# Kernel optimization log

Measured on AMD Instinct MI355X. Metric: run time of the kernel, lower is better.

## Reference

```python
import jax, jax.numpy as jnp
import numpy as np

HIDDEN = 768
HEAD = 64


def setup_inputs() -> dict:
    key = jax.random.key(0)
    ks = jax.random.split(key, 9)
    s = 1.0 / np.sqrt(HIDDEN)
    so = 1.0 / np.sqrt(HEAD)
    return {
        "x": jax.random.normal(ks[0], (4, 4096, HIDDEN), dtype=jnp.float32),
        "Wq": jax.random.uniform(ks[1], (HIDDEN, HEAD), jnp.float32, -s, s),
        "bq": jax.random.uniform(ks[2], (HEAD,), jnp.float32, -s, s),
        "Wk": jax.random.uniform(ks[3], (HIDDEN, HEAD), jnp.float32, -s, s),
        "bk": jax.random.uniform(ks[4], (HEAD,), jnp.float32, -s, s),
        "Wv": jax.random.uniform(ks[5], (HIDDEN, HEAD), jnp.float32, -s, s),
        "bv": jax.random.uniform(ks[6], (HEAD,), jnp.float32, -s, s),
        "Wo": jax.random.uniform(ks[7], (HEAD, HIDDEN), jnp.float32, -so, so),
        "bo": jax.random.uniform(ks[8], (HIDDEN,), jnp.float32, -so, so),
    }


def reference(x, Wq, bq, Wk, bk, Wv, bv, Wo, bo):
    # x: [b, s, h]
    q = jnp.einsum('bsh,hd->bsd', x, Wq) + bq  # [b, s, d]
    k = jnp.einsum('bsh,hd->bsd', x, Wk) + bk
    v = jnp.einsum('bsh,hd->bsd', x, Wv) + bv
    scale = 1.0 / jnp.sqrt(jnp.asarray(HEAD, x.dtype))
    scores = jnp.einsum('bqd,bkd->bqk', q, k) * scale  # [b, s, s]
    A = jax.nn.softmax(scores, axis=-1)
    ctx = jnp.einsum('bqk,bkd->bqd', A, v)  # [b, s, d]
    return jnp.einsum('bsd,dh->bsh', ctx, Wo) + bo
```

## Files before the change

kernel.cpp:

```cpp
#include <hip/hip_runtime.h>
#include <hip/hip_bf16.h>
#include <stdint.h>

#define BB 4
#define SS 4096
#define HH 768
#define DD 64

typedef __attribute__((ext_vector_type(8))) short bf16x8;
typedef __attribute__((ext_vector_type(4))) short bf16x4;
typedef __attribute__((ext_vector_type(4))) float f32x4;
typedef __attribute__((ext_vector_type(2))) float f32x2;
typedef __attribute__((ext_vector_type(16))) float f32x16;
typedef __attribute__((ext_vector_type(4))) uint32_t u32x4;
typedef __attribute__((ext_vector_type(2))) uint32_t u32x2;

typedef const __attribute__((address_space(1))) uint32_t g_u32;
typedef __attribute__((address_space(3))) uint32_t l_u32;
#define ASYNC16(gp, lp) \
  __builtin_amdgcn_global_load_lds((g_u32*)(gp), (l_u32*)(lp), 16, 0, 0)

__device__ __forceinline__ short f2bf(float f) {
  uint32_t u = __builtin_bit_cast(uint32_t, f);
  u += 0x7fffu + ((u >> 16) & 1u);
  return (short)(u >> 16);
}

#define QSCALE 0.18033688011112042f

__global__ __launch_bounds__(256) void prep_kernel(
    const float* __restrict__ Wq, const float* __restrict__ bq,
    const float* __restrict__ Wk, const float* __restrict__ bk,
    const float* __restrict__ Wv, const float* __restrict__ bv,
    const float* __restrict__ Wo,
    short* __restrict__ wqkvF, float* __restrict__ bqkv,
    short* __restrict__ woF) {
  int idx = blockIdx.x * 256 + threadIdx.x;
  const int N1 = 192 * HH;
  const int N2 = HH * DD;
  if (idx < N1) {
    int n = idx / HH, k = idx % HH;
    float v;
    if (n < 64)       v = Wq[k * 64 + n] * QSCALE;
    else if (n < 128) v = Wk[k * 64 + (n - 64)];
    else              v = Wv[k * 64 + (n - 128)];
    int tile = (n >> 4) * 24 + (k >> 5);
    int lane = (((k >> 3) & 3) << 4) | (n & 15);
    wqkvF[tile * 512 + lane * 8 + (k & 7)] = f2bf(v);
  } else if (idx < N1 + N2) {
    int j = idx - N1;
    int n = j / 64, k = j % 64;
    int tile = (n >> 4) * 2 + (k >> 5);
    int lane = (((k >> 3) & 3) << 4) | (n & 15);
    woF[tile * 512 + lane * 8 + (k & 7)] = f2bf(Wo[k * HH + n]);
  } else if (idx < N1 + N2 + 192) {
    int n = idx - N1 - N2;
    float v;
    if (n < 64)       v = bq[n] * QSCALE;
    else if (n < 128) v = bk[n - 64];
    else              v = bv[n - 128];
    bqkv[n] = v;
  }
}

__global__ __launch_bounds__(256, 2) void qkv_kernel(
    const float* __restrict__ x, const short* __restrict__ wF,
    const float* __restrict__ bqkv,
    short* __restrict__ qb, short* __restrict__ kb, short* __restrict__ vT) {
  __shared__ short xl[32 * 776];
  __shared__ short vtile[64 * 32];
  const int tid = threadIdx.x;
  const int w = tid >> 6, lane = tid & 63, g = (lane >> 4) & 3, n16 = lane & 15;
  const int m0 = blockIdx.x * 32;

  const float4* xsrc = (const float4*)&x[m0 * HH];
#pragma unroll
  for (int i = 0; i < 24; ++i) {
    int idx = i * 256 + tid;
    const float4 f = xsrc[idx];
    int elem = idx * 4;
    int row = elem / HH, col = elem % HH;
    bf16x4 p = { f2bf(f.x), f2bf(f.y), f2bf(f.z), f2bf(f.w) };
    *(bf16x4*)&xl[row * 776 + col] = p;
  }
  __syncthreads();

  f32x4 acc[2][3] = {};
  const short* wbase = &wF[w * 36864 + lane * 8];

#pragma unroll 2
  for (int kc = 0; kc < 24; ++kc) {
    const int ko = kc * 32 + g * 8;
    bf16x8 a0 = *(const bf16x8*)&xl[n16 * 776 + ko];
    bf16x8 a1 = *(const bf16x8*)&xl[(16 + n16) * 776 + ko];
    bf16x8 b0 = *(const bf16x8*)&wbase[kc * 512];
    bf16x8 b1 = *(const bf16x8*)&wbase[12288 + kc * 512];
    bf16x8 b2 = *(const bf16x8*)&wbase[24576 + kc * 512];
    acc[0][0] = __builtin_amdgcn_mfma_f32_16x16x32_bf16(a0, b0, acc[0][0], 0, 0, 0);
    acc[1][0] = __builtin_amdgcn_mfma_f32_16x16x32_bf16(a1, b0, acc[1][0], 0, 0, 0);
    acc[0][1] = __builtin_amdgcn_mfma_f32_16x16x32_bf16(a0, b1, acc[0][1], 0, 0, 0);
    acc[1][1] = __builtin_amdgcn_mfma_f32_16x16x32_bf16(a1, b1, acc[1][1], 0, 0, 0);
    acc[0][2] = __builtin_amdgcn_mfma_f32_16x16x32_bf16(a0, b2, acc[0][2], 0, 0, 0);
    acc[1][2] = __builtin_amdgcn_mfma_f32_16x16x32_bf16(a1, b2, acc[1][2], 0, 0, 0);
  }

#pragma unroll
  for (int ct = 0; ct < 3; ++ct) {
    int nG = w * 48 + ct * 16 + n16;
    float bias = bqkv[nG];
    if (nG < 128) {
#pragma unroll
      for (int rt = 0; rt < 2; ++rt)
#pragma unroll
        for (int r = 0; r < 4; ++r) {
          int rowg = m0 + rt * 16 + g * 4 + r;
          short val = f2bf(acc[rt][ct][r] + bias);
          if (nG < 64) qb[rowg * 64 + nG] = val;
          else         kb[rowg * 64 + (nG - 64)] = val;
        }
    } else {
      int d = nG - 128;
#pragma unroll
      for (int rt = 0; rt < 2; ++rt) {
        bf16x4 p = { f2bf(acc[rt][ct][0] + bias), f2bf(acc[rt][ct][1] + bias),
                     f2bf(acc[rt][ct][2] + bias), f2bf(acc[rt][ct][3] + bias) };
        *(bf16x4*)&vtile[d * 32 + rt * 16 + g * 4] = p;
      }
    }
  }

  __syncthreads();
  {
    int d = tid >> 2, part = tid & 3;
    bf16x8 o = *(const bf16x8*)&vtile[d * 32 + part * 8];
    int b = m0 >> 12;
    *(bf16x8*)&vT[(b * 64 + d) * SS + (m0 & 4095) + part * 8] = o;
  }
}

__global__ __launch_bounds__(256, 2) void flash_kernel(
    const short* __restrict__ qb, const short* __restrict__ kb,
    const short* __restrict__ vT,
    float* __restrict__ Opart, float* __restrict__ lpart) {
  __shared__ short Kl[2][128 * 64];
  __shared__ short Vl[2][64 * 128];
  __shared__ float l_lds[64];
  const int tid = threadIdx.x;
  const int w = tid >> 6, lane = tid & 63;
  const int m31 = lane & 31, h = lane >> 5;
  const int qt32 = w & 1, kh = w >> 1;
  const int part = blockIdx.x, rg = part >> 1, sp = part & 1;
  const int b = rg >> 6, qt = rg & 63;
  const short* qB = qb + (b * SS + qt * 64 + qt32 * 32) * DD;
  const short* kB = kb + (b * SS + sp * 2048) * DD;
  const short* vB = vT + b * DD * SS + sp * 2048;

  int srcK[4], srcV[4];
#pragma unroll
  for (int i = 0; i < 4; ++i) {
    int rowK = (w * 4 + i) * 8 + (lane >> 3);
    srcK[i] = rowK * 64 + (((lane & 7) ^ (rowK & 7)) << 3);
    int dV = (w * 4 + i) * 4 + (lane >> 4);
    srcV[i] = dV * SS + (((lane & 15) ^ (dV & 15)) << 3);
  }

  bf16x8 aQ[4];
#pragma unroll
  for (int kk = 0; kk < 4; ++kk)
    aQ[kk] = *(const bf16x8*)&qB[m31 * DD + kk * 16 + 8 * h];

  f32x16 oacc[2] = {};
  float l_run = 0.f;

#pragma unroll
  for (int i = 0; i < 4; ++i) {
    ASYNC16(kB + srcK[i], &Kl[0][(w * 4 + i) * 512]);
    ASYNC16(vB + srcV[i], &Vl[0][(w * 4 + i) * 512]);
  }

  for (int kt = 0; kt < 16; ++kt) {
    const int cur = kt & 1;
    if (kt < 15) {
      const short* kN = kB + (kt + 1) * 8192;
      const short* vN = vB + (kt + 1) * 128;
#pragma unroll
      for (int i = 0; i < 4; ++i) {
        ASYNC16(kN + srcK[i], &Kl[cur ^ 1][(w * 4 + i) * 512]);
        ASYNC16(vN + srcV[i], &Vl[cur ^ 1][(w * 4 + i) * 512]);
      }
      asm volatile("s_waitcnt vmcnt(8)" ::: "memory");
    } else {
      asm volatile("s_waitcnt vmcnt(0)" ::: "memory");
    }
    __builtin_amdgcn_s_barrier();
    __builtin_amdgcn_sched_barrier(0);

#pragma unroll
    for (int kt2 = 0; kt2 < 2; ++kt2) {
      f32x16 sc = {};
      const int r = kh * 64 + kt2 * 32 + m31;
      const int rx = r & 7;
      __builtin_amdgcn_s_setprio(1);
#pragma unroll
      for (int kk = 0; kk < 4; ++kk) {
        bf16x8 aK = *(const bf16x8*)&Kl[cur][r * 64 + ((((kk << 1) | h) ^ rx) << 3)];
        sc = __builtin_amdgcn_mfma_f32_32x32x16_bf16(aK, aQ[kk], sc, 0, 0, 0);
      }
      __builtin_amdgcn_s_setprio(0);

      f32x2 ls2 = {0.f, 0.f};
      uint32_t pp[8];
#pragma unroll
      for (int j = 0; j < 8; ++j) {
        uint32_t ea = __builtin_bit_cast(uint32_t,
                        __builtin_amdgcn_exp2f(sc[2 * j]));
        uint32_t eb = __builtin_bit_cast(uint32_t,
                        __builtin_amdgcn_exp2f(sc[2 * j + 1]));
        f32x2 t = { __builtin_bit_cast(float, ea & 0xffff0000u),
                    __builtin_bit_cast(float, eb & 0xffff0000u) };
        ls2 += t;
        pp[j] = __builtin_amdgcn_perm(eb, ea, 0x07060302u);
      }
      l_run += ls2.x + ls2.y;

      u32x2 r02 = __builtin_amdgcn_permlane32_swap(pp[0], pp[2], false, false);
      u32x2 r13 = __builtin_amdgcn_permlane32_swap(pp[1], pp[3], false, false);
      u32x2 r46 = __builtin_amdgcn_permlane32_swap(pp[4], pp[6], false, false);
      u32x2 r57 = __builtin_amdgcn_permlane32_swap(pp[5], pp[7], false, false);

#pragma unroll
      for (int s = 0; s < 2; ++s) {
        u32x4 fr = (s == 0) ? u32x4{r02.x, r13.x, r02.y, r13.y}
                            : u32x4{r46.x, r57.x, r46.y, r57.y};
        bf16x8 aP = __builtin_bit_cast(bf16x8, fr);
        const int cv = (kh << 3) | (kt2 << 2) | (s << 1) | h;
        __builtin_amdgcn_s_setprio(1);
#pragma unroll
        for (int dt = 0; dt < 2; ++dt) {
          const int rv = dt * 32 + m31;
          bf16x8 bV = *(const bf16x8*)&Vl[cur][rv * 128 + ((cv ^ (rv & 15)) << 3)];
          oacc[dt] = __builtin_amdgcn_mfma_f32_32x32x16_bf16(aP, bV, oacc[dt], 0, 0, 0);
        }
        __builtin_amdgcn_s_setprio(0);
      }
    }
    __builtin_amdgcn_sched_barrier(0);
    __builtin_amdgcn_s_barrier();
  }

  l_run += __shfl_xor(l_run, 32);

  __syncthreads();
  float* sO = (float*)&Kl[0][0];
  if (kh == 1) {
#pragma unroll
    for (int dt = 0; dt < 2; ++dt)
#pragma unroll
      for (int r = 0; r < 16; ++r) {
        int q = (r & 3) + 8 * (r >> 2) + 4 * h;
        sO[qt32 * 2048 + q * 64 + dt * 32 + m31] = oacc[dt][r];
      }
    if (lane < 32) l_lds[qt32 * 32 + lane] = l_run;
  }
  __syncthreads();
  if (kh == 0) {
#pragma unroll
    for (int dt = 0; dt < 2; ++dt)
#pragma unroll
      for (int r = 0; r < 16; ++r) {
        int q = (r & 3) + 8 * (r >> 2) + 4 * h;
        float o = oacc[dt][r] + sO[qt32 * 2048 + q * 64 + dt * 32 + m31];
        Opart[(part * 64 + qt32 * 32 + q) * 64 + dt * 32 + m31] = o;
      }
    if (lane < 32)
      lpart[part * 64 + qt32 * 32 + lane] = l_run + l_lds[qt32 * 32 + lane];
  }
}

__global__ __launch_bounds__(256, 4) void proj_kernel(
    const float* __restrict__ Opart, const float* __restrict__ lpart,
    const short* __restrict__ woF, const float* __restrict__ bo,
    float* __restrict__ out) {
  const int tid = threadIdx.x;
  const int w = tid >> 6, lane = tid & 63, g = lane >> 4, n16 = lane & 15;
  const int m0 = blockIdx.x * 16;
  const int colbase = w * 192;

  const int row = m0 + n16;
  const int rg = row >> 6, r64 = row & 63;
  float lsum = lpart[(rg * 2 + 0) * 64 + r64] + lpart[(rg * 2 + 1) * 64 + r64];
  float inv = 1.f / lsum;

  bf16x8 aC[2];
#pragma unroll
  for (int kk = 0; kk < 2; ++kk) {
    const int d0 = kk * 32 + g * 8;
    float s0 = 0, s1 = 0, s2 = 0, s3 = 0, s4 = 0, s5 = 0, s6 = 0, s7 = 0;
#pragma unroll
    for (int sp = 0; sp < 2; ++sp) {
      const float* op = &Opart[((rg * 2 + sp) * 64 + r64) * 64 + d0];
      const float4 v0 = *(const float4*)&op[0];
      const float4 v1 = *(const float4*)&op[4];
      s0 += v0.x; s1 += v0.y; s2 += v0.z; s3 += v0.w;
      s4 += v1.x; s5 += v1.y; s6 += v1.z; s7 += v1.w;
    }
    aC[kk] = bf16x8{ f2bf(s0 * inv), f2bf(s1 * inv), f2bf(s2 * inv), f2bf(s3 * inv),
                     f2bf(s4 * inv), f2bf(s5 * inv), f2bf(s6 * inv), f2bf(s7 * inv) };
  }

  const short* wbase = &woF[w * 12288 + lane * 8];

  f32x4 acc[12] = {};
#pragma unroll
  for (int kk = 0; kk < 2; ++kk) {
#pragma unroll
    for (int ct = 0; ct < 12; ++ct) {
      bf16x8 bW = *(const bf16x8*)&wbase[(ct * 2 + kk) * 512];
      acc[ct] = __builtin_amdgcn_mfma_f32_16x16x32_bf16(aC[kk], bW, acc[ct], 0, 0, 0);
    }
  }
#pragma unroll
  for (int ct = 0; ct < 12; ++ct) {
    int nG = colbase + ct * 16 + n16;
    float bias = bo[nG];
#pragma unroll
    for (int r = 0; r < 4; ++r) {
      int rowg = m0 + g * 4 + r;
      out[rowg * HH + nG] = acc[ct][r] + bias;
    }
  }
}

extern "C" void kernel_launch(void* const* d_in, const int* in_sizes, int n_in,
                              void* d_out, int out_size, void* d_ws, size_t ws_size,
                              hipStream_t stream) {
  const float* x  = (const float*)d_in[0];
  const float* Wq = (const float*)d_in[1];
  const float* bq = (const float*)d_in[2];
  const float* Wk = (const float*)d_in[3];
  const float* bk = (const float*)d_in[4];
  const float* Wv = (const float*)d_in[5];
  const float* bv = (const float*)d_in[6];
  const float* Wo = (const float*)d_in[7];
  const float* bo = (const float*)d_in[8];
  float* out = (float*)d_out;

  char* ws = (char*)d_ws;
  short* qb    = (short*)(ws + 0);
  short* kb    = (short*)(ws + (2u << 20));
  short* vT    = (short*)(ws + (4u << 20));
  short* wqkvF = (short*)(ws + (6u << 20));
  short* woF   = (short*)(ws + (6u << 20) + 384 * 1024);
  float* bqkv  = (float*)(ws + (6u << 20) + 512 * 1024);
  float* lpart = (float*)(ws + (7u << 20));
  float* Opart = (float*)(ws + (8u << 20));

  hipLaunchKernelGGL(prep_kernel, dim3(769), dim3(256), 0, stream,
                     Wq, bq, Wk, bk, Wv, bv, Wo, wqkvF, bqkv, woF);
  hipLaunchKernelGGL(qkv_kernel, dim3(512), dim3(256), 0, stream,
                     x, wqkvF, bqkv, qb, kb, vT);
  hipLaunchKernelGGL(flash_kernel, dim3(512), dim3(256), 0, stream,
                     qb, kb, vT, Opart, lpart);
  hipLaunchKernelGGL(proj_kernel, dim3(1024), dim3(256), 0, stream,
                     Opart, lpart, woF, bo, out);
}
```

Baseline: 158.9 us.

## Fuse split-KV flash attention and output projection into one 512-thread kernel

Both KV halves of each 64-query tile now run as eight waves inside one 512-thread block, instead of two separate blocks. Their partial outputs and row sums are combined through LDS atomics, normalized, and converted to bf16. The Wo projection then runs in the same kernel, which drops the Opart/lpart global round trip and the separate proj_kernel launch. In exchange there are half as many blocks (256) with one block per CU, twice the LDS per block, and LDS atomic adds during the reduction.

```diff
diff --git a/kernel.cpp b/kernel.cpp
--- a/kernel.cpp
+++ b/kernel.cpp
@@ -138,18 +138,18 @@
   }
 }
 
-__global__ __launch_bounds__(256, 2) void flash_kernel(
+__global__ __launch_bounds__(512, 1) void flash_kernel(
     const short* __restrict__ qb, const short* __restrict__ kb,
-    const short* __restrict__ vT,
-    float* __restrict__ Opart, float* __restrict__ lpart) {
-  __shared__ short Kl[2][128 * 64];
-  __shared__ short Vl[2][64 * 128];
-  __shared__ float l_lds[64];
+    const short* __restrict__ vT, const short* __restrict__ woF,
+    const float* __restrict__ bo, float* __restrict__ out) {
+  __shared__ short Kl[2][2][8192];
+  __shared__ short Vl[2][2][8192];
+  __shared__ float lA[64];
   const int tid = threadIdx.x;
   const int w = tid >> 6, lane = tid & 63;
   const int m31 = lane & 31, h = lane >> 5;
-  const int qt32 = w & 1, kh = w >> 1;
-  const int part = blockIdx.x, rg = part >> 1, sp = part & 1;
+  const int qt32 = w & 1, kh = (w >> 1) & 1, sp = w >> 2, wl = w & 3;
+  const int rg = blockIdx.x;
   const int b = rg >> 6, qt = rg & 63;
   const short* qB = qb + (b * SS + qt * 64 + qt32 * 32) * DD;
   const short* kB = kb + (b * SS + sp * 2048) * DD;
@@ -158,9 +158,9 @@
   int srcK[4], srcV[4];
 #pragma unroll
   for (int i = 0; i < 4; ++i) {
-    int rowK = (w * 4 + i) * 8 + (lane >> 3);
+    int rowK = (wl * 4 + i) * 8 + (lane >> 3);
     srcK[i] = rowK * 64 + (((lane & 7) ^ (rowK & 7)) << 3);
-    int dV = (w * 4 + i) * 4 + (lane >> 4);
+    int dV = (wl * 4 + i) * 4 + (lane >> 4);
     srcV[i] = dV * SS + (((lane & 15) ^ (dV & 15)) << 3);
   }
 
@@ -174,8 +174,8 @@
 
 #pragma unroll
   for (int i = 0; i < 4; ++i) {
-    ASYNC16(kB + srcK[i], &Kl[0][(w * 4 + i) * 512]);
-    ASYNC16(vB + srcV[i], &Vl[0][(w * 4 + i) * 512]);
+    ASYNC16(kB + srcK[i], &Kl[sp][0][(wl * 4 + i) * 512]);
+    ASYNC16(vB + srcV[i], &Vl[sp][0][(wl * 4 + i) * 512]);
   }
 
   for (int kt = 0; kt < 16; ++kt) {
@@ -185,8 +185,8 @@
       const short* vN = vB + (kt + 1) * 128;
 #pragma unroll
       for (int i = 0; i < 4; ++i) {
-        ASYNC16(kN + srcK[i], &Kl[cur ^ 1][(w * 4 + i) * 512]);
-        ASYNC16(vN + srcV[i], &Vl[cur ^ 1][(w * 4 + i) * 512]);
+        ASYNC16(kN + srcK[i], &Kl[sp][cur ^ 1][(wl * 4 + i) * 512]);
+        ASYNC16(vN + srcV[i], &Vl[sp][cur ^ 1][(wl * 4 + i) * 512]);
       }
       asm volatile("s_waitcnt vmcnt(8)" ::: "memory");
     } else {
@@ -203,7 +203,7 @@
       __builtin_amdgcn_s_setprio(1);
 #pragma unroll
       for (int kk = 0; kk < 4; ++kk) {
-        bf16x8 aK = *(const bf16x8*)&Kl[cur][r * 64 + ((((kk << 1) | h) ^ rx) << 3)];
+        bf16x8 aK = *(const bf16x8*)&Kl[sp][cur][r * 64 + ((((kk << 1) | h) ^ rx) << 3)];
         sc = __builtin_amdgcn_mfma_f32_32x32x16_bf16(aK, aQ[kk], sc, 0, 0, 0);
       }
       __builtin_amdgcn_s_setprio(0);
@@ -238,7 +238,7 @@
 #pragma unroll
         for (int dt = 0; dt < 2; ++dt) {
           const int rv = dt * 32 + m31;
-          bf16x8 bV = *(const bf16x8*)&Vl[cur][rv * 128 + ((cv ^ (rv & 15)) << 3)];
+          bf16x8 bV = *(const bf16x8*)&Vl[sp][cur][rv * 128 + ((cv ^ (rv & 15)) << 3)];
           oacc[dt] = __builtin_amdgcn_mfma_f32_32x32x16_bf16(aP, bV, oacc[dt], 0, 0, 0);
         }
         __builtin_amdgcn_s_setprio(0);
@@ -250,83 +250,73 @@
 
   l_run += __shfl_xor(l_run, 32);
 
-  __syncthreads();
-  float* sO = (float*)&Kl[0][0];
-  if (kh == 1) {
+  float* ctxA = (float*)&Kl[0][0][0];
+  short* ctxB = &Kl[1][0][0];
+  if (sp == 0 && kh == 0) {
 #pragma unroll
     for (int dt = 0; dt < 2; ++dt)
 #pragma unroll
       for (int r = 0; r < 16; ++r) {
         int q = (r & 3) + 8 * (r >> 2) + 4 * h;
-        sO[qt32 * 2048 + q * 64 + dt * 32 + m31] = oacc[dt][r];
-      }
-    if (lane < 32) l_lds[qt32 * 32 + lane] = l_run;
-  }
-  __syncthreads();
-  if (kh == 0) {
+        ctxA[(qt32 * 32 + q) * 64 + dt * 32 + m31] = oacc[dt][r];
+      }
+    if (lane < 32) lA[qt32 * 32 + lane] = l_run;
+  }
+  __syncthreads();
+  if (!(sp == 0 && kh == 0)) {
 #pragma unroll
     for (int dt = 0; dt < 2; ++dt)
 #pragma unroll
       for (int r = 0; r < 16; ++r) {
         int q = (r & 3) + 8 * (r >> 2) + 4 * h;
-        float o = oacc[dt][r] + sO[qt32 * 2048 + q * 64 + dt * 32 + m31];
-        Opart[(part * 64 + qt32 * 32 + q) * 64 + dt * 32 + m31] = o;
-      }
-    if (lane < 32)
-      lpart[part * 64 + qt32 * 32 + lane] = l_run + l_lds[qt32 * 32 + lane];
-  }
-}
-
-__global__ __launch_bounds__(256, 4) void proj_kernel(
-    const float* __restrict__ Opart, const float* __restrict__ lpart,
-    const short* __restrict__ woF, const float* __restrict__ bo,
-    float* __restrict__ out) {
-  const int tid = threadIdx.x;
-  const int w = tid >> 6, lane = tid & 63, g = lane >> 4, n16 = lane & 15;
-  const int m0 = blockIdx.x * 16;
-  const int colbase = w * 192;
-
-  const int row = m0 + n16;
-  const int rg = row >> 6, r64 = row & 63;
-  float lsum = lpart[(rg * 2 + 0) * 64 + r64] + lpart[(rg * 2 + 1) * 64 + r64];
-  float inv = 1.f / lsum;
-
-  bf16x8 aC[2];
-#pragma unroll
-  for (int kk = 0; kk < 2; ++kk) {
-    const int d0 = kk * 32 + g * 8;
-    float s0 = 0, s1 = 0, s2 = 0, s3 = 0, s4 = 0, s5 = 0, s6 = 0, s7 = 0;
-#pragma unroll
-    for (int sp = 0; sp < 2; ++sp) {
-      const float* op = &Opart[((rg * 2 + sp) * 64 + r64) * 64 + d0];
-      const float4 v0 = *(const float4*)&op[0];
-      const float4 v1 = *(const float4*)&op[4];
-      s0 += v0.x; s1 += v0.y; s2 += v0.z; s3 += v0.w;
-      s4 += v1.x; s5 += v1.y; s6 += v1.z; s7 += v1.w;
-    }
-    aC[kk] = bf16x8{ f2bf(s0 * inv), f2bf(s1 * inv), f2bf(s2 * inv), f2bf(s3 * inv),
-                     f2bf(s4 * inv), f2bf(s5 * inv), f2bf(s6 * inv), f2bf(s7 * inv) };
-  }
-
-  const short* wbase = &woF[w * 12288 + lane * 8];
-
-  f32x4 acc[12] = {};
-#pragma unroll
-  for (int kk = 0; kk < 2; ++kk) {
-#pragma unroll
-    for (int ct = 0; ct < 12; ++ct) {
-      bf16x8 bW = *(const bf16x8*)&wbase[(ct * 2 + kk) * 512];
-      acc[ct] = __builtin_amdgcn_mfma_f32_16x16x32_bf16(aC[kk], bW, acc[ct], 0, 0, 0);
-    }
-  }
-#pragma unroll
-  for (int ct = 0; ct < 12; ++ct) {
-    int nG = colbase + ct * 16 + n16;
-    float bias = bo[nG];
-#pragma unroll
-    for (int r = 0; r < 4; ++r) {
-      int rowg = m0 + g * 4 + r;
-      out[rowg * HH + nG] = acc[ct][r] + bias;
+        atomicAdd(&ctxA[(qt32 * 32 + q) * 64 + dt * 32 + m31], oacc[dt][r]);
+      }
+    if (lane < 32) atomicAdd(&lA[qt32 * 32 + lane], l_run);
+  }
+  __syncthreads();
+  {
+    int q = tid >> 3, d0 = (tid & 7) * 8;
+    float inv = 1.f / lA[q];
+    const float4 v0 = *(const float4*)&ctxA[q * 64 + d0];
+    const float4 v1 = *(const float4*)&ctxA[q * 64 + d0 + 4];
+    bf16x8 p = { f2bf(v0.x * inv), f2bf(v0.y * inv),
+                 f2bf(v0.z * inv), f2bf(v0.w * inv),
+                 f2bf(v1.x * inv), f2bf(v1.y * inv),
+                 f2bf(v1.z * inv), f2bf(v1.w * inv) };
+    *(bf16x8*)&ctxB[q * 72 + d0] = p;
+  }
+  __syncthreads();
+
+  {
+    const int g = lane >> 4, n16 = lane & 15;
+    bf16x8 bW[12];
+#pragma unroll
+    for (int ct = 0; ct < 6; ++ct)
+#pragma unroll
+      for (int kk = 0; kk < 2; ++kk)
+        bW[ct * 2 + kk] =
+            *(const bf16x8*)&woF[((w * 6 + ct) * 2 + kk) * 512 + lane * 8];
+    const int rowbase = b * SS + qt * 64;
+#pragma unroll
+    for (int rt = 0; rt < 4; ++rt) {
+      bf16x8 a0 = *(const bf16x8*)&ctxB[(rt * 16 + n16) * 72 + g * 8];
+      bf16x8 a1 = *(const bf16x8*)&ctxB[(rt * 16 + n16) * 72 + g * 8 + 32];
+      f32x4 acc[6] = {};
+#pragma unroll
+      for (int ct = 0; ct < 6; ++ct) {
+        acc[ct] = __builtin_amdgcn_mfma_f32_16x16x32_bf16(a0, bW[ct * 2], acc[ct], 0, 0, 0);
+        acc[ct] = __builtin_amdgcn_mfma_f32_16x16x32_bf16(a1, bW[ct * 2 + 1], acc[ct], 0, 0, 0);
+      }
+#pragma unroll
+      for (int ct = 0; ct < 6; ++ct) {
+        int nG = w * 96 + ct * 16 + n16;
+        float bias = bo[nG];
+#pragma unroll
+        for (int r = 0; r < 4; ++r) {
+          int rowg = rowbase + rt * 16 + g * 4 + r;
+          out[rowg * HH + nG] = acc[ct][r] + bias;
+        }
+      }
     }
   }
 }
@@ -352,15 +342,11 @@
   short* wqkvF = (short*)(ws + (6u << 20));
   short* woF   = (short*)(ws + (6u << 20) + 384 * 1024);
   float* bqkv  = (float*)(ws + (6u << 20) + 512 * 1024);
-  float* lpart = (float*)(ws + (7u << 20));
-  float* Opart = (float*)(ws + (8u << 20));
 
   hipLaunchKernelGGL(prep_kernel, dim3(769), dim3(256), 0, stream,
                      Wq, bq, Wk, bk, Wv, bv, Wo, wqkvF, bqkv, woF);
   hipLaunchKernelGGL(qkv_kernel, dim3(512), dim3(256), 0, stream,
                      x, wqkvF, bqkv, qb, kb, vT);
-  hipLaunchKernelGGL(flash_kernel, dim3(512), dim3(256), 0, stream,
-                     qb, kb, vT, Opart, lpart);
-  hipLaunchKernelGGL(proj_kernel, dim3(1024), dim3(256), 0, stream,
-                     Opart, lpart, woF, bo, out);
-}
+  hipLaunchKernelGGL(flash_kernel, dim3(256), dim3(512), 0, stream,
+                     qb, kb, vT, woF, bo, out);
+}
```

After: 172.4 us. 1.09x slower.

## Fuse output projection into flash kernel via last-block atomic counter

Applied to the files above, without the earlier changes.

Removes the separate projection kernel. Each row group's two key-split blocks increment an atomic counter, and the block that finishes last combines the partial outputs, normalizes them, and runs the Wo projection into the output. The counters are zeroed in the prep kernel. This saves a kernel launch and the reread of the partials in a separate pass, at the cost of threadfences, an atomic per block, and projection work concentrated in half of the flash blocks.

```diff
diff --git a/kernel.cpp b/kernel.cpp
--- a/kernel.cpp
+++ b/kernel.cpp
@@ -34,7 +34,7 @@
     const float* __restrict__ Wv, const float* __restrict__ bv,
     const float* __restrict__ Wo,
     short* __restrict__ wqkvF, float* __restrict__ bqkv,
-    short* __restrict__ woF) {
+    short* __restrict__ woF, int* __restrict__ cnt) {
   int idx = blockIdx.x * 256 + threadIdx.x;
   const int N1 = 192 * HH;
   const int N2 = HH * DD;
@@ -60,6 +60,8 @@
     else if (n < 128) v = bk[n - 64];
     else              v = bv[n - 128];
     bqkv[n] = v;
+  } else if (idx < N1 + N2 + 192 + 256) {
+    cnt[idx - N1 - N2 - 192] = 0;
   }
 }
 
@@ -141,10 +143,13 @@
 __global__ __launch_bounds__(256, 2) void flash_kernel(
     const short* __restrict__ qb, const short* __restrict__ kb,
     const short* __restrict__ vT,
-    float* __restrict__ Opart, float* __restrict__ lpart) {
+    float* __restrict__ Opart, float* __restrict__ lpart,
+    const short* __restrict__ woF, const float* __restrict__ bo,
+    float* __restrict__ out, int* __restrict__ cnt) {
   __shared__ short Kl[2][128 * 64];
   __shared__ short Vl[2][64 * 128];
   __shared__ float l_lds[64];
+  __shared__ int lastS;
   const int tid = threadIdx.x;
   const int w = tid >> 6, lane = tid & 63;
   const int m31 = lane & 31, h = lane >> 5;
@@ -275,58 +280,61 @@
     if (lane < 32)
       lpart[part * 64 + qt32 * 32 + lane] = l_run + l_lds[qt32 * 32 + lane];
   }
-}
-
-__global__ __launch_bounds__(256, 4) void proj_kernel(
-    const float* __restrict__ Opart, const float* __restrict__ lpart,
-    const short* __restrict__ woF, const float* __restrict__ bo,
-    float* __restrict__ out) {
-  const int tid = threadIdx.x;
-  const int w = tid >> 6, lane = tid & 63, g = lane >> 4, n16 = lane & 15;
-  const int m0 = blockIdx.x * 16;
-  const int colbase = w * 192;
-
-  const int row = m0 + n16;
-  const int rg = row >> 6, r64 = row & 63;
-  float lsum = lpart[(rg * 2 + 0) * 64 + r64] + lpart[(rg * 2 + 1) * 64 + r64];
-  float inv = 1.f / lsum;
-
-  bf16x8 aC[2];
-#pragma unroll
-  for (int kk = 0; kk < 2; ++kk) {
-    const int d0 = kk * 32 + g * 8;
-    float s0 = 0, s1 = 0, s2 = 0, s3 = 0, s4 = 0, s5 = 0, s6 = 0, s7 = 0;
-#pragma unroll
-    for (int sp = 0; sp < 2; ++sp) {
-      const float* op = &Opart[((rg * 2 + sp) * 64 + r64) * 64 + d0];
-      const float4 v0 = *(const float4*)&op[0];
-      const float4 v1 = *(const float4*)&op[4];
-      s0 += v0.x; s1 += v0.y; s2 += v0.z; s3 += v0.w;
-      s4 += v1.x; s5 += v1.y; s6 += v1.z; s7 += v1.w;
-    }
-    aC[kk] = bf16x8{ f2bf(s0 * inv), f2bf(s1 * inv), f2bf(s2 * inv), f2bf(s3 * inv),
-                     f2bf(s4 * inv), f2bf(s5 * inv), f2bf(s6 * inv), f2bf(s7 * inv) };
-  }
-
-  const short* wbase = &woF[w * 12288 + lane * 8];
-
-  f32x4 acc[12] = {};
-#pragma unroll
-  for (int kk = 0; kk < 2; ++kk) {
-#pragma unroll
-    for (int ct = 0; ct < 12; ++ct) {
-      bf16x8 bW = *(const bf16x8*)&wbase[(ct * 2 + kk) * 512];
-      acc[ct] = __builtin_amdgcn_mfma_f32_16x16x32_bf16(aC[kk], bW, acc[ct], 0, 0, 0);
-    }
-  }
-#pragma unroll
-  for (int ct = 0; ct < 12; ++ct) {
-    int nG = colbase + ct * 16 + n16;
-    float bias = bo[nG];
-#pragma unroll
-    for (int r = 0; r < 4; ++r) {
-      int rowg = m0 + g * 4 + r;
-      out[rowg * HH + nG] = acc[ct][r] + bias;
+
+  __threadfence();
+  if (tid == 0) lastS = atomicAdd(&cnt[rg], 1);
+  __syncthreads();
+  if (lastS != 1) return;
+  __threadfence();
+
+  short* ctxB = &Kl[1][0];
+  {
+    int q = tid >> 2, d0 = (tid & 3) * 16;
+    float inv = 1.f / (lpart[(rg * 2 + 0) * 64 + q] +
+                       lpart[(rg * 2 + 1) * 64 + q]);
+    const float* o0 = &Opart[((rg * 2 + 0) * 64 + q) * 64 + d0];
+    const float* o1 = &Opart[((rg * 2 + 1) * 64 + q) * 64 + d0];
+#pragma unroll
+    for (int c = 0; c < 2; ++c) {
+      const float4 a0 = *(const float4*)&o0[c * 8];
+      const float4 a1 = *(const float4*)&o0[c * 8 + 4];
+      const float4 b0 = *(const float4*)&o1[c * 8];
+      const float4 b1 = *(const float4*)&o1[c * 8 + 4];
+      bf16x8 p = { f2bf((a0.x + b0.x) * inv), f2bf((a0.y + b0.y) * inv),
+                   f2bf((a0.z + b0.z) * inv), f2bf((a0.w + b0.w) * inv),
+                   f2bf((a1.x + b1.x) * inv), f2bf((a1.y + b1.y) * inv),
+                   f2bf((a1.z + b1.z) * inv), f2bf((a1.w + b1.w) * inv) };
+      *(bf16x8*)&ctxB[q * 72 + d0 + c * 8] = p;
+    }
+  }
+  __syncthreads();
+
+  {
+    const int g = lane >> 4, n16 = lane & 15;
+    const short* wbase = &woF[w * 12288 + lane * 8];
+    const int rowbase = b * SS + qt * 64;
+#pragma unroll
+    for (int rt = 0; rt < 4; ++rt) {
+      bf16x8 a0 = *(const bf16x8*)&ctxB[(rt * 16 + n16) * 72 + g * 8];
+      bf16x8 a1 = *(const bf16x8*)&ctxB[(rt * 16 + n16) * 72 + g * 8 + 32];
+      f32x4 acc[12] = {};
+#pragma unroll
+      for (int ct = 0; ct < 12; ++ct) {
+        bf16x8 bW0 = *(const bf16x8*)&wbase[(ct * 2 + 0) * 512];
+        bf16x8 bW1 = *(const bf16x8*)&wbase[(ct * 2 + 1) * 512];
+        acc[ct] = __builtin_amdgcn_mfma_f32_16x16x32_bf16(a0, bW0, acc[ct], 0, 0, 0);
+        acc[ct] = __builtin_amdgcn_mfma_f32_16x16x32_bf16(a1, bW1, acc[ct], 0, 0, 0);
+      }
+#pragma unroll
+      for (int ct = 0; ct < 12; ++ct) {
+        int nG = w * 192 + ct * 16 + n16;
+        float bias = bo[nG];
+#pragma unroll
+        for (int r = 0; r < 4; ++r) {
+          int rowg = rowbase + rt * 16 + g * 4 + r;
+          out[rowg * HH + nG] = acc[ct][r] + bias;
+        }
+      }
     }
   }
 }
@@ -352,15 +360,14 @@
   short* wqkvF = (short*)(ws + (6u << 20));
   short* woF   = (short*)(ws + (6u << 20) + 384 * 1024);
   float* bqkv  = (float*)(ws + (6u << 20) + 512 * 1024);
+  int*   cnt   = (int*)(ws + (6u << 20) + 516 * 1024);
   float* lpart = (float*)(ws + (7u << 20));
   float* Opart = (float*)(ws + (8u << 20));
 
-  hipLaunchKernelGGL(prep_kernel, dim3(769), dim3(256), 0, stream,
-                     Wq, bq, Wk, bk, Wv, bv, Wo, wqkvF, bqkv, woF);
+  hipLaunchKernelGGL(prep_kernel, dim3(770), dim3(256), 0, stream,
+                     Wq, bq, Wk, bk, Wv, bv, Wo, wqkvF, bqkv, woF, cnt);
   hipLaunchKernelGGL(qkv_kernel, dim3(512), dim3(256), 0, stream,
                      x, wqkvF, bqkv, qb, kb, vT);
   hipLaunchKernelGGL(flash_kernel, dim3(512), dim3(256), 0, stream,
-                     qb, kb, vT, Opart, lpart);
-  hipLaunchKernelGGL(proj_kernel, dim3(1024), dim3(256), 0, stream,
-                     Opart, lpart, woF, bo, out);
-}
+                     qb, kb, vT, Opart, lpart, woF, bo, out, cnt);
+}
```

After: 244.3 us. 1.54x slower.

## Give each wave its own query rows and split keys four ways across blocks

Applied to the files above, without the earlier changes.

The flash kernel previously split each block's 128-key tile between two wave pairs, which meant an LDS reduction of the partial outputs at the end. Now each block covers 128 query rows, one 32-row slice per wave, and every wave walks all keys in the tile. The key range is split into four partitions of 1024 keys across blocks instead of two of 2048. This removes the intra-block LDS combine and barriers and doubles query reuse of each loaded K/V tile. In exchange the fp32 partial output buffer doubles and the projection kernel has to sum four partials per row instead of two.

```diff
diff --git a/kernel.cpp b/kernel.cpp
--- a/kernel.cpp
+++ b/kernel.cpp
@@ -144,16 +144,14 @@
     float* __restrict__ Opart, float* __restrict__ lpart) {
   __shared__ short Kl[2][128 * 64];
   __shared__ short Vl[2][64 * 128];
-  __shared__ float l_lds[64];
   const int tid = threadIdx.x;
   const int w = tid >> 6, lane = tid & 63;
   const int m31 = lane & 31, h = lane >> 5;
-  const int qt32 = w & 1, kh = w >> 1;
-  const int part = blockIdx.x, rg = part >> 1, sp = part & 1;
-  const int b = rg >> 6, qt = rg & 63;
-  const short* qB = qb + (b * SS + qt * 64 + qt32 * 32) * DD;
-  const short* kB = kb + (b * SS + sp * 2048) * DD;
-  const short* vB = vT + b * DD * SS + sp * 2048;
+  const int part = blockIdx.x, rg = part >> 2, sp = part & 3;
+  const int b = rg >> 5, qt = rg & 31;
+  const short* qB = qb + (b * SS + qt * 128 + w * 32) * DD;
+  const short* kB = kb + (b * SS + sp * 1024) * DD;
+  const short* vB = vT + b * DD * SS + sp * 1024;
 
   int srcK[4], srcV[4];
 #pragma unroll
@@ -178,9 +176,9 @@
     ASYNC16(vB + srcV[i], &Vl[0][(w * 4 + i) * 512]);
   }
 
-  for (int kt = 0; kt < 16; ++kt) {
+  for (int kt = 0; kt < 8; ++kt) {
     const int cur = kt & 1;
-    if (kt < 15) {
+    if (kt < 7) {
       const short* kN = kB + (kt + 1) * 8192;
       const short* vN = vB + (kt + 1) * 128;
 #pragma unroll
@@ -196,9 +194,9 @@
     __builtin_amdgcn_sched_barrier(0);
 
 #pragma unroll
-    for (int kt2 = 0; kt2 < 2; ++kt2) {
+    for (int kt2 = 0; kt2 < 4; ++kt2) {
       f32x16 sc = {};
-      const int r = kh * 64 + kt2 * 32 + m31;
+      const int r = kt2 * 32 + m31;
       const int rx = r & 7;
       __builtin_amdgcn_s_setprio(1);
 #pragma unroll
@@ -233,7 +231,7 @@
         u32x4 fr = (s == 0) ? u32x4{r02.x, r13.x, r02.y, r13.y}
                             : u32x4{r46.x, r57.x, r46.y, r57.y};
         bf16x8 aP = __builtin_bit_cast(bf16x8, fr);
-        const int cv = (kh << 3) | (kt2 << 2) | (s << 1) | h;
+        const int cv = (kt2 << 2) | (s << 1) | h;
         __builtin_amdgcn_s_setprio(1);
 #pragma unroll
         for (int dt = 0; dt < 2; ++dt) {
@@ -249,32 +247,14 @@
   }
 
   l_run += __shfl_xor(l_run, 32);
-
-  __syncthreads();
-  float* sO = (float*)&Kl[0][0];
-  if (kh == 1) {
-#pragma unroll
-    for (int dt = 0; dt < 2; ++dt)
-#pragma unroll
-      for (int r = 0; r < 16; ++r) {
-        int q = (r & 3) + 8 * (r >> 2) + 4 * h;
-        sO[qt32 * 2048 + q * 64 + dt * 32 + m31] = oacc[dt][r];
-      }
-    if (lane < 32) l_lds[qt32 * 32 + lane] = l_run;
-  }
-  __syncthreads();
-  if (kh == 0) {
-#pragma unroll
-    for (int dt = 0; dt < 2; ++dt)
-#pragma unroll
-      for (int r = 0; r < 16; ++r) {
-        int q = (r & 3) + 8 * (r >> 2) + 4 * h;
-        float o = oacc[dt][r] + sO[qt32 * 2048 + q * 64 + dt * 32 + m31];
-        Opart[(part * 64 + qt32 * 32 + q) * 64 + dt * 32 + m31] = o;
-      }
-    if (lane < 32)
-      lpart[part * 64 + qt32 * 32 + lane] = l_run + l_lds[qt32 * 32 + lane];
-  }
+#pragma unroll
+  for (int dt = 0; dt < 2; ++dt)
+#pragma unroll
+    for (int r = 0; r < 16; ++r) {
+      int q = (r & 3) + 8 * (r >> 2) + 4 * h;
+      Opart[(part * 128 + w * 32 + q) * 64 + dt * 32 + m31] = oacc[dt][r];
+    }
+  if (lane < 32) lpart[part * 128 + w * 32 + lane] = l_run;
 }
 
 __global__ __launch_bounds__(256, 4) void proj_kernel(
@@ -287,8 +267,9 @@
   const int colbase = w * 192;
 
   const int row = m0 + n16;
-  const int rg = row >> 6, r64 = row & 63;
-  float lsum = lpart[(rg * 2 + 0) * 64 + r64] + lpart[(rg * 2 + 1) * 64 + r64];
+  const int key = row >> 7, r128 = row & 127;
+  float lsum = lpart[(key * 4 + 0) * 128 + r128] + lpart[(key * 4 + 1) * 128 + r128] +
+               lpart[(key * 4 + 2) * 128 + r128] + lpart[(key * 4 + 3) * 128 + r128];
   float inv = 1.f / lsum;
 
   bf16x8 aC[2];
@@ -297,8 +278,8 @@
     const int d0 = kk * 32 + g * 8;
     float s0 = 0, s1 = 0, s2 = 0, s3 = 0, s4 = 0, s5 = 0, s6 = 0, s7 = 0;
 #pragma unroll
-    for (int sp = 0; sp < 2; ++sp) {
-      const float* op = &Opart[((rg * 2 + sp) * 64 + r64) * 64 + d0];
+    for (int sp = 0; sp < 4; ++sp) {
+      const float* op = &Opart[((key * 4 + sp) * 128 + r128) * 64 + d0];
       const float4 v0 = *(const float4*)&op[0];
       const float4 v1 = *(const float4*)&op[4];
       s0 += v0.x; s1 += v0.y; s2 += v0.z; s3 += v0.w;
```

New measurement: 159.0 us. About the same (+0.1%).
